# Kernel optimization log

Measured on AMD Instinct MI355X. Metric: run time of the kernel, lower is better.

## Reference

```python
import jax, jax.numpy as jnp
import numpy as np

H = 16        # num_attention_heads
D = 128       # head_dim
HID = 2048    # hidden_size
S = 2048      # seq_len
B = 2
EPS = 1.1920928955078125e-07  # torch.finfo(float32).eps, F.rms_norm default


def _rope(x, cos, sin):
    # x: [B,H,S,D]; cos/sin: [S, D//2] broadcast over B,H
    d = x.shape[-1] // 2
    x1, x2 = x[..., :d], x[..., d:]
    return jnp.concatenate([x1 * cos + x2 * sin, -x1 * sin + x2 * cos], axis=-1)


def _rmsnorm(x):
    ms = jnp.mean(x * x, axis=-1, keepdims=True)
    return x * jax.lax.rsqrt(ms + EPS)


def setup_inputs() -> dict:
    key = jax.random.key(0)
    ks = jax.random.split(key, 7)
    x = jax.random.normal(ks[0], (B, S, HID), dtype=jnp.float32)
    cos = jax.random.uniform(ks[1], (S, D // 2), dtype=jnp.float32)
    sin = jax.random.uniform(ks[2], (S, D // 2), dtype=jnp.float32)
    sc = 1.0 / np.sqrt(HID)
    wq = jax.random.normal(ks[3], (H * D, HID), dtype=jnp.float32) * sc
    wk = jax.random.normal(ks[4], (D, HID), dtype=jnp.float32) * sc  # num_kv_heads=1
    wv = jax.random.normal(ks[5], (D, HID), dtype=jnp.float32) * sc
    wo = jax.random.normal(ks[6], (HID, H * D), dtype=jnp.float32) * sc
    return {"x": x, "cos": cos, "sin": sin, "wq": wq, "wk": wk, "wv": wv, "wo": wo}


def reference(x, cos, sin, wq, wk, wv, wo):
    b, s, _ = x.shape
    # projections
    q = (x @ wq.T).reshape(b, s, H, D).transpose(0, 2, 1, 3)        # [b,H,s,D]
    k = (x @ wk.T).reshape(b, s, 1, D).transpose(0, 2, 1, 3)        # [b,1,s,D] MQA
    v = (x @ wv.T).reshape(b, s, 1, D).transpose(0, 2, 1, 3)
    # RoPE then RMS-norm on q/k (keep k/v in MQA [b,1,s,D]; broadcasting replaces expand)
    q = _rmsnorm(_rope(q, cos, sin))
    k = _rmsnorm(_rope(k, cos, sin))
    # causal attention
    scores = jnp.einsum('bhqd,bgkd->bhqk', q, k) * (D ** -0.5)      # [b,H,s,s]
    mask = jnp.tril(jnp.ones((s, s), dtype=bool))
    scores = jnp.where(mask, scores, -jnp.inf)
    attn = jax.nn.softmax(scores, axis=-1)
    out = jnp.einsum('bhqk,bgkd->bhqd', attn, v)                    # [b,H,s,D]
    out = out.transpose(0, 2, 1, 3).reshape(b, s, H * D)
    return out @ wo.T
```

## Files before the change

### kernel.cpp

```cpp
#include <hip/hip_runtime.h>
#include <hip/hip_bf16.h>

typedef __attribute__((ext_vector_type(8))) short bf16x8;
typedef __attribute__((ext_vector_type(4))) float f32x4;

constexpr int cH = 16, cD = 128, cHID = 2048, cS = 2048, cB = 2;
constexpr float cEPS = 1.1920928955078125e-07f;
constexpr float cQS = 0.08838834764831845f * 1.442695040888963f;

__device__ __forceinline__ unsigned short f2bf(float f) {
  union { float f; unsigned u; } v; v.f = f;
  unsigned r = v.u + 0x7fffu + ((v.u >> 16) & 1u);
  return (unsigned short)(r >> 16);
}
__device__ __forceinline__ unsigned pk2(float a, float b) {
  return (unsigned)f2bf(a) | ((unsigned)f2bf(b) << 16);
}
__device__ __forceinline__ f32x4 mfma16(bf16x8 a, bf16x8 b, f32x4 c) {
  return __builtin_amdgcn_mfma_f32_16x16x32_bf16(a, b, c, 0, 0, 0);
}
__device__ __forceinline__ void gl2l(const void* g, void* l) {
  __builtin_amdgcn_global_load_lds(
      (const __attribute__((address_space(1))) unsigned int*)g,
      (__attribute__((address_space(3))) unsigned int*)l, 16, 0, 0);
}

__global__ __launch_bounds__(256) void cvt_all(
    const float* __restrict__ x, const float* __restrict__ wq,
    const float* __restrict__ wk, const float* __restrict__ wv,
    const float* __restrict__ wo,
    unsigned short* __restrict__ xb, unsigned short* __restrict__ wqb,
    unsigned short* __restrict__ wkb, unsigned short* __restrict__ wvb,
    unsigned short* __restrict__ wob)
{
  long i = (long)blockIdx.x * 2048 + threadIdx.x * 8;
  const float* s; unsigned short* d; long off;
  if (i < 8388608)       { s = x;  d = xb;  off = i; }
  else if (i < 12582912) { s = wq; d = wqb; off = i - 8388608; }
  else if (i < 12845056) { s = wk; d = wkb; off = i - 12582912; }
  else if (i < 13107200) { s = wv; d = wvb; off = i - 12845056; }
  else                   { s = wo; d = wob; off = i - 13107200; }
  float4 v0 = *reinterpret_cast<const float4*>(s + off);
  float4 v1 = *reinterpret_cast<const float4*>(s + off + 4);
  uint4 o; o.x = pk2(v0.x, v0.y); o.y = pk2(v0.z, v0.w);
  o.z = pk2(v1.x, v1.y); o.w = pk2(v1.z, v1.w);
  *reinterpret_cast<uint4*>(d + off) = o;
}

__global__ __launch_bounds__(256) void gemm_qkv(
    const unsigned short* __restrict__ A,
    const unsigned short* __restrict__ Wq,
    const unsigned short* __restrict__ Wk,
    const unsigned short* __restrict__ Wv,
    const float* __restrict__ cosb, const float* __restrict__ sinb,
    unsigned short* __restrict__ Qn,
    unsigned short* __restrict__ Kn,
    unsigned short* __restrict__ Vn)
{
  __shared__ unsigned short lds[8192];
  const int t = threadIdx.x;
  const int bm = blockIdx.x, bn = blockIdx.y;
  const int lane = t & 63, w = t >> 6;
  const int hi = lane >> 4, l15 = lane & 15;

  const unsigned short* Wp; long wbase;
  if (bn < 16)       { Wp = Wq; wbase = (long)bn * 128; }
  else if (bn == 16) { Wp = Wk; wbase = 0; }
  else               { Wp = Wv; wbase = 0; }

  f32x4 acc[2][8] = {};

  for (int k0 = 0; k0 < 2048; k0 += 32) {
    #pragma unroll
    for (int i = 0; i < 2; ++i) {
      int c = w + 4 * i;
      gl2l(A + (long)(bm * 128 + 16 * c + (lane >> 2)) * 2048 + k0 + (lane & 3) * 8,
           &lds[c * 512]);
      gl2l(Wp + (wbase + 16 * c + (lane >> 2)) * 2048 + k0 + (lane & 3) * 8,
           &lds[4096 + c * 512]);
    }
    __syncthreads();
    bf16x8 af[2], bff[8];
    #pragma unroll
    for (int m = 0; m < 2; ++m)
      af[m] = *reinterpret_cast<const bf16x8*>(&lds[(w * 32 + m * 16 + l15) * 32 + hi * 8]);
    #pragma unroll
    for (int n = 0; n < 8; ++n)
      bff[n] = *reinterpret_cast<const bf16x8*>(&lds[4096 + (n * 16 + l15) * 32 + hi * 8]);
    #pragma unroll
    for (int m = 0; m < 2; ++m)
      #pragma unroll
      for (int n = 0; n < 8; ++n)
        acc[m][n] = mfma16(af[m], bff[n], acc[m][n]);
    __syncthreads();
  }

  const int rowbase = bm * 128 + w * 32;
  if (bn == 17) {
    #pragma unroll
    for (int m = 0; m < 2; ++m)
      #pragma unroll
      for (int r = 0; r < 4; ++r) {
        int grow = rowbase + m * 16 + hi * 4 + r;
        int b = grow >> 11, s = grow & 2047;
        long base = ((long)b * cS + s) * cD;
        #pragma unroll
        for (int n = 0; n < 8; ++n)
          Vn[base + n * 16 + l15] = f2bf(acc[m][n][r]);
      }
  } else {
    #pragma unroll
    for (int m = 0; m < 2; ++m)
      #pragma unroll
      for (int r = 0; r < 4; ++r) {
        int grow = rowbase + m * 16 + hi * 4 + r;
        int b = grow >> 11, s = grow & 2047;
        float o1[4], o2[4], ss = 0.f;
        #pragma unroll
        for (int n = 0; n < 4; ++n) {
          float cv = cosb[(long)s * 64 + n * 16 + l15];
          float sv = sinb[(long)s * 64 + n * 16 + l15];
          float x1 = acc[m][n][r], x2 = acc[m][n + 4][r];
          o1[n] = x1 * cv + x2 * sv;
          o2[n] = x2 * cv - x1 * sv;
          ss += o1[n] * o1[n] + o2[n] * o2[n];
        }
        ss += __shfl_xor(ss, 1); ss += __shfl_xor(ss, 2);
        ss += __shfl_xor(ss, 4); ss += __shfl_xor(ss, 8);
        float scn = rsqrtf(ss * (1.0f / 128.0f) + cEPS);
        if (bn < 16) {
          float sq = scn * cQS;
          long base = (((long)b * cH + bn) * cS + s) * cD;
          #pragma unroll
          for (int n = 0; n < 4; ++n) {
            Qn[base + n * 16 + l15] = f2bf(o1[n] * sq);
            Qn[base + 64 + n * 16 + l15] = f2bf(o2[n] * sq);
          }
        } else {
          long base = ((long)b * cS + s) * cD;
          int xs = (s & 7) << 3;
          #pragma unroll
          for (int n = 0; n < 4; ++n) {
            Kn[base + ((n * 16 + l15) ^ xs)] = f2bf(o1[n] * scn);
            Kn[base + (((64 + n * 16 + l15)) ^ xs)] = f2bf(o2[n] * scn);
          }
        }
      }
  }
}

__global__ __launch_bounds__(256) void vtrans(
    const unsigned short* __restrict__ Vn, unsigned short* __restrict__ Vt)
{
  __shared__ unsigned short Tl[64][72];
  const int t = threadIdx.x;
  const int st = blockIdx.x * 64, dt = blockIdx.y * 64, b = blockIdx.z;
  const unsigned short* Vb = Vn + (long)b * cS * cD;
  #pragma unroll
  for (int i = 0; i < 2; ++i) {
    int r = i * 32 + (t >> 3), c8 = (t & 7) * 8;
    *reinterpret_cast<uint4*>(&Tl[r][c8]) =
        *reinterpret_cast<const uint4*>(&Vb[(long)(st + r) * cD + dt + c8]);
  }
  __syncthreads();
  unsigned short* Vo = Vt + (long)b * cD * cS;
  #pragma unroll
  for (int i = 0; i < 2; ++i) {
    int d = i * 32 + (t >> 3), sb = (t & 7) * 8;
    unsigned short e[8];
    #pragma unroll
    for (int j = 0; j < 8; ++j) e[j] = Tl[sb + j][d];
    uint4 o;
    o.x = (unsigned)e[0] | ((unsigned)e[1] << 16);
    o.y = (unsigned)e[2] | ((unsigned)e[3] << 16);
    o.z = (unsigned)e[4] | ((unsigned)e[5] << 16);
    o.w = (unsigned)e[6] | ((unsigned)e[7] << 16);
    int dg = dt + d;
    *reinterpret_cast<uint4*>(&Vo[(long)dg * cS + st + (sb ^ ((dg & 7) << 3))]) = o;
  }
}

__global__ __launch_bounds__(256) void attn2(
    const unsigned short* __restrict__ Qn,
    const unsigned short* __restrict__ Kn,
    const unsigned short* __restrict__ Vt,
    unsigned short* __restrict__ O)
{
  __shared__ unsigned short lds[32768];
  const int t = threadIdx.x, w = t >> 6, lane = t & 63;
  const int hi = lane >> 4, l15 = lane & 15;
  const int h = blockIdx.y, b = blockIdx.z;
  const unsigned short* Qb = Qn + (long)(b * cH + h) * cS * cD;
  const unsigned short* Kb = Kn + (long)b * cS * cD;
  const unsigned short* Vtb = Vt + (long)b * cD * cS;
  const int x3 = (l15 & 7) << 3;

  union OU { unsigned u[4]; bf16x8 v; };
  OU ou; ou.u[0] = ou.u[1] = ou.u[2] = ou.u[3] = 0x3F803F80u;
  const bf16x8 onesv = ou.v;

  #pragma unroll 1
  for (int pass = 0; pass < 2; ++pass) {
    const int qt = (pass == 0) ? blockIdx.x : 31 - blockIdx.x;
    const int q0 = qt * 64;
    const int qrow = q0 + w * 16 + l15;
    const int nt = qt + 1;

    bf16x8 qf[4];
    #pragma unroll
    for (int kc = 0; kc < 4; ++kc)
      qf[kc] = *reinterpret_cast<const bf16x8*>(&Qb[(long)qrow * cD + kc * 32 + hi * 8]);

    const unsigned short* kp = Kb + (long)(16 * w + (lane >> 4)) * cD + (lane & 15) * 8;
    const unsigned short* vp[4];
    #pragma unroll
    for (int i = 0; i < 4; ++i)
      vp[i] = Vtb + (long)(32 * w + 8 * i + (lane >> 3)) * cS + (lane & 7) * 8;

    auto STAGE = [&](int buf) {
      unsigned short* kd = &lds[buf * 8192 + w * 2048];
      unsigned short* vd = &lds[16384 + buf * 8192 + w * 2048];
      #pragma unroll
      for (int i = 0; i < 4; ++i) {
        gl2l(kp + i * 512, kd + i * 512);
        gl2l(vp[i], vd + i * 512);
      }
      kp += 8192;
      #pragma unroll
      for (int i = 0; i < 4; ++i) vp[i] += 64;
    };

    f32x4 oacc[8] = {};
    f32x4 lacc = {};
    float mrun = -1e30f;

    STAGE(0);
    int cur = 0;

    #pragma unroll 1
    for (int kt = 0; kt < nt; ++kt) {
      const int kv0 = kt * 64;
      if (kt + 1 < nt) {
        STAGE(cur ^ 1);
        asm volatile("s_waitcnt vmcnt(8)" ::: "memory");
      } else {
        asm volatile("s_waitcnt vmcnt(0)" ::: "memory");
      }
      __builtin_amdgcn_s_barrier();
      __builtin_amdgcn_sched_barrier(0);

      const unsigned short* kbase = &lds[cur * 8192];
      const unsigned short* vbase = &lds[16384 + cur * 8192];

      f32x4 st[4] = {};
      #pragma unroll
      for (int kc = 0; kc < 4; ++kc) {
        #pragma unroll
        for (int n = 0; n < 4; ++n) {
          bf16x8 kf = *reinterpret_cast<const bf16x8*>(
              &kbase[(n * 16 + l15) * 128 + ((kc * 32 + hi * 8) ^ x3)]);
          st[n] = mfma16(kf, qf[kc], st[n]);
        }
      }

      float p[4][4];
      if (kt == qt) {
        #pragma unroll
        for (int n = 0; n < 4; ++n)
          #pragma unroll
          for (int r = 0; r < 4; ++r) {
            int kv = kv0 + n * 16 + hi * 4 + r;
            p[n][r] = (kv <= qrow) ? st[n][r] : -1e30f;
          }
      } else {
        #pragma unroll
        for (int n = 0; n < 4; ++n)
          #pragma unroll
          for (int r = 0; r < 4; ++r)
            p[n][r] = st[n][r];
      }

      float pmax = p[0][0];
      #pragma unroll
      for (int n = 0; n < 4; ++n)
        #pragma unroll
        for (int r = 0; r < 4; ++r) pmax = fmaxf(pmax, p[n][r]);
      pmax = fmaxf(pmax, __shfl_xor(pmax, 16));
      pmax = fmaxf(pmax, __shfl_xor(pmax, 32));

      if (!__all(pmax - mrun <= 8.0f)) {
        float mnew = fmaxf(mrun, pmax);
        float alpha = exp2f(mrun - mnew);
        mrun = mnew;
        #pragma unroll
        for (int n = 0; n < 8; ++n)
          #pragma unroll
          for (int r = 0; r < 4; ++r) oacc[n][r] *= alpha;
        #pragma unroll
        for (int r = 0; r < 4; ++r) lacc[r] *= alpha;
      }

      #pragma unroll
      for (int n = 0; n < 4; ++n)
        #pragma unroll
        for (int r = 0; r < 4; ++r)
          p[n][r] = exp2f(p[n][r] - mrun);

      unsigned pkl[4], pkh[4];
      #pragma unroll
      for (int n = 0; n < 4; ++n) {
        pkl[n] = pk2(p[n][0], p[n][1]);
        pkh[n] = pk2(p[n][2], p[n][3]);
      }

      bf16x8 pa[2];
      #pragma unroll
      for (int c = 0; c < 2; ++c) {
        int ns = 2 * c + (hi >> 1);
        int no = 2 * c + ((hi >> 1) ^ 1);
        unsigned own0 = pkl[ns], own1 = pkh[ns];
        unsigned ot0 = pkl[no], ot1 = pkh[no];
        unsigned a160 = __shfl_xor(own0, 16), a161 = __shfl_xor(own1, 16);
        unsigned a320 = __shfl_xor(ot0, 32),  a321 = __shfl_xor(ot1, 32);
        unsigned a480 = __shfl_xor(ot0, 48),  a481 = __shfl_xor(ot1, 48);
        unsigned w0 = hi == 0 ? own0 : hi == 1 ? a480 : hi == 2 ? a320 : a160;
        unsigned w1 = hi == 0 ? own1 : hi == 1 ? a481 : hi == 2 ? a321 : a161;
        unsigned w2 = hi == 0 ? a160 : hi == 1 ? a320 : hi == 2 ? a480 : own0;
        unsigned w3 = hi == 0 ? a161 : hi == 1 ? a321 : hi == 2 ? a481 : own1;
        union { unsigned u[4]; bf16x8 v; } cvt;
        cvt.u[0] = w0; cvt.u[1] = w1; cvt.u[2] = w2; cvt.u[3] = w3;
        pa[c] = cvt.v;
      }

      #pragma unroll
      for (int c = 0; c < 2; ++c) lacc = mfma16(onesv, pa[c], lacc);
      #pragma unroll
      for (int n2 = 0; n2 < 8; ++n2) {
        #pragma unroll
        for (int c = 0; c < 2; ++c) {
          bf16x8 vf = *reinterpret_cast<const bf16x8*>(
              &vbase[(n2 * 16 + l15) * 64 + ((c * 32 + hi * 8) ^ x3)]);
          oacc[n2] = mfma16(vf, pa[c], oacc[n2]);
        }
      }
      __builtin_amdgcn_s_barrier();
      cur ^= 1;
    }

    {
      float inv = 1.0f / lacc[0];
      unsigned short* Ol = &lds[w * 2176];
      #pragma unroll
      for (int n2 = 0; n2 < 8; ++n2)
        #pragma unroll
        for (int r = 0; r < 4; ++r)
          Ol[l15 * 136 + n2 * 16 + hi * 4 + r] = f2bf(oacc[n2][r] * inv);
      __syncthreads();
      #pragma unroll
      for (int i = 0; i < 4; ++i) {
        int row = hi + 4 * i;
        uint4 ov = *reinterpret_cast<const uint4*>(&Ol[row * 136 + l15 * 8]);
        *reinterpret_cast<uint4*>(
            &O[(long)(b * cS + q0 + w * 16 + row) * (cH * cD) + h * cD + l15 * 8]) = ov;
      }
      __syncthreads();
    }
  }
}

__global__ __launch_bounds__(256) void gemm_out(
    const unsigned short* __restrict__ A,
    const unsigned short* __restrict__ W,
    float* __restrict__ C)
{
  __shared__ unsigned short lds[8192];
  const int t = threadIdx.x;
  const int bm = blockIdx.x, bn = blockIdx.y;
  const int lane = t & 63, w = t >> 6;
  const int wr = w >> 1, wc = w & 1, hi = lane >> 4, l15 = lane & 15;
  const long wbase = (long)bn * 128;

  f32x4 acc[4][4] = {};
  for (int k0 = 0; k0 < 2048; k0 += 32) {
    #pragma unroll
    for (int i = 0; i < 2; ++i) {
      int c = w + 4 * i;
      gl2l(A + (long)(bm * 128 + 16 * c + (lane >> 2)) * 2048 + k0 + (lane & 3) * 8,
           &lds[c * 512]);
      gl2l(W + (wbase + 16 * c + (lane >> 2)) * 2048 + k0 + (lane & 3) * 8,
           &lds[4096 + c * 512]);
    }
    __syncthreads();
    bf16x8 af[4], bff[4];
    #pragma unroll
    for (int m = 0; m < 4; ++m)
      af[m] = *reinterpret_cast<const bf16x8*>(&lds[(wr * 64 + m * 16 + l15) * 32 + hi * 8]);
    #pragma unroll
    for (int n = 0; n < 4; ++n)
      bff[n] = *reinterpret_cast<const bf16x8*>(&lds[4096 + (wc * 64 + n * 16 + l15) * 32 + hi * 8]);
    #pragma unroll
    for (int m = 0; m < 4; ++m)
      #pragma unroll
      for (int n = 0; n < 4; ++n)
        acc[m][n] = mfma16(af[m], bff[n], acc[m][n]);
    __syncthreads();
  }

  #pragma unroll
  for (int m = 0; m < 4; ++m) {
    int row = bm * 128 + wr * 64 + m * 16 + hi * 4;
    #pragma unroll
    for (int n = 0; n < 4; ++n) {
      int col = bn * 128 + wc * 64 + n * 16 + l15;
      #pragma unroll
      for (int r = 0; r < 4; ++r)
        C[(long)(row + r) * 2048 + col] = acc[m][n][r];
    }
  }
}

extern "C" void kernel_launch(void* const* d_in, const int* in_sizes, int n_in,
                              void* d_out, int out_size, void* d_ws, size_t ws_size,
                              hipStream_t stream) {
  const float* x    = (const float*)d_in[0];
  const float* cosb = (const float*)d_in[1];
  const float* sinb = (const float*)d_in[2];
  const float* wq   = (const float*)d_in[3];
  const float* wk   = (const float*)d_in[4];
  const float* wv   = (const float*)d_in[5];
  const float* wo   = (const float*)d_in[6];
  float* out = (float*)d_out;

  char* ws = (char*)d_ws;
  unsigned short* xb  = (unsigned short*)(ws);
  unsigned short* wqb = (unsigned short*)(ws + 16777216);
  unsigned short* wkb = (unsigned short*)(ws + 25165824);
  unsigned short* wvb = (unsigned short*)(ws + 25690112);
  unsigned short* Qn  = (unsigned short*)(ws + 26214400);
  unsigned short* Kn  = (unsigned short*)(ws + 42991616);
  unsigned short* Vn  = (unsigned short*)(ws + 44040192);
  unsigned short* Vtg = (unsigned short*)(ws + 45088768);
  unsigned short* wob = (unsigned short*)(ws + 46137344);
  unsigned short* Ob  = (unsigned short*)ws;

  cvt_all<<<dim3(8448), 256, 0, stream>>>(x, wq, wk, wv, wo, xb, wqb, wkb, wvb, wob);
  gemm_qkv<<<dim3(32, 18), 256, 0, stream>>>(xb, wqb, wkb, wvb, cosb, sinb, Qn, Kn, Vn);
  vtrans<<<dim3(32, 2, 2), 256, 0, stream>>>(Vn, Vtg);
  attn2<<<dim3(16, 16, 2), 256, 0, stream>>>(Qn, Kn, Vtg, Ob);
  gemm_out<<<dim3(32, 16), 256, 0, stream>>>(Ob, wob, out);
}
```

Measured before the change: 207.1 us.

## Use 16x16x16 bf16 MFMA for PV to skip P cross-lane shuffles

Replaces the PV and row-sum MFMAs with the K=16 bf16 variant so the softmax probabilities already held in each lane's score layout can feed the MFMA directly, removing the shuffle-and-select exchange of packed P. Packs P with the hardware v_cvt_pk_bf16_f32 instruction instead of software rounding. Also defers the cross-lane max reduction to the rescale branch and raises wave priority around the MFMA blocks. Doubles the MFMA instruction count for PV with smaller V fragment loads, and the deferred max changes which max is used per lane only when rescaling is skipped.

```diff
diff --git a/kernel.cpp b/kernel.cpp
--- a/kernel.cpp
+++ b/kernel.cpp
@@ -2,6 +2,7 @@
 #include <hip/hip_bf16.h>
 
 typedef __attribute__((ext_vector_type(8))) short bf16x8;
+typedef __attribute__((ext_vector_type(4))) short bf16x4;
 typedef __attribute__((ext_vector_type(4))) float f32x4;
 
 constexpr int cH = 16, cD = 128, cHID = 2048, cS = 2048, cB = 2;
@@ -16,8 +17,23 @@
 __device__ __forceinline__ unsigned pk2(float a, float b) {
   return (unsigned)f2bf(a) | ((unsigned)f2bf(b) << 16);
 }
+__device__ __forceinline__ unsigned cvtpk(float a, float b) {
+  unsigned r;
+  asm("v_cvt_pk_bf16_f32 %0, %1, %2" : "=v"(r) : "v"(a), "v"(b));
+  return r;
+}
 __device__ __forceinline__ f32x4 mfma16(bf16x8 a, bf16x8 b, f32x4 c) {
   return __builtin_amdgcn_mfma_f32_16x16x32_bf16(a, b, c, 0, 0, 0);
+}
+__device__ __forceinline__ f32x4 mfma16k16(bf16x4 a, bf16x4 b, f32x4 c) {
+#if __has_builtin(__builtin_amdgcn_mfma_f32_16x16x16bf16_1k)
+  return __builtin_amdgcn_mfma_f32_16x16x16bf16_1k(a, b, c, 0, 0, 0);
+#else
+  f32x4 d;
+  asm volatile("v_mfma_f32_16x16x16_bf16 %0, %1, %2, %3\n\ts_nop 7\n\ts_nop 2"
+               : "=v"(d) : "v"(a), "v"(b), "v"(c));
+  return d;
+#endif
 }
 __device__ __forceinline__ void gl2l(const void* g, void* l) {
   __builtin_amdgcn_global_load_lds(
@@ -195,9 +211,9 @@
   const unsigned short* Vtb = Vt + (long)b * cD * cS;
   const int x3 = (l15 & 7) << 3;
 
-  union OU { unsigned u[4]; bf16x8 v; };
-  OU ou; ou.u[0] = ou.u[1] = ou.u[2] = ou.u[3] = 0x3F803F80u;
-  const bf16x8 onesv = ou.v;
+  union O4 { unsigned u[2]; bf16x4 v; };
+  O4 o4; o4.u[0] = o4.u[1] = 0x3F803F80u;
+  const bf16x4 ones4 = o4.v;
 
   #pragma unroll 1
   for (int pass = 0; pass < 2; ++pass) {
@@ -253,6 +269,7 @@
       const unsigned short* vbase = &lds[16384 + cur * 8192];
 
       f32x4 st[4] = {};
+      __builtin_amdgcn_s_setprio(1);
       #pragma unroll
       for (int kc = 0; kc < 4; ++kc) {
         #pragma unroll
@@ -262,6 +279,7 @@
           st[n] = mfma16(kf, qf[kc], st[n]);
         }
       }
+      __builtin_amdgcn_s_setprio(0);
 
       float p[4][4];
       if (kt == qt) {
@@ -280,15 +298,15 @@
             p[n][r] = st[n][r];
       }
 
-      float pmax = p[0][0];
-      #pragma unroll
-      for (int n = 0; n < 4; ++n)
-        #pragma unroll
-        for (int r = 0; r < 4; ++r) pmax = fmaxf(pmax, p[n][r]);
-      pmax = fmaxf(pmax, __shfl_xor(pmax, 16));
-      pmax = fmaxf(pmax, __shfl_xor(pmax, 32));
+      float t0 = fmaxf(fmaxf(p[0][0], p[0][1]), fmaxf(p[0][2], p[0][3]));
+      float t1 = fmaxf(fmaxf(p[1][0], p[1][1]), fmaxf(p[1][2], p[1][3]));
+      float t2 = fmaxf(fmaxf(p[2][0], p[2][1]), fmaxf(p[2][2], p[2][3]));
+      float t3 = fmaxf(fmaxf(p[3][0], p[3][1]), fmaxf(p[3][2], p[3][3]));
+      float pmax = fmaxf(fmaxf(t0, t1), fmaxf(t2, t3));
 
       if (!__all(pmax - mrun <= 8.0f)) {
+        pmax = fmaxf(pmax, __shfl_xor(pmax, 16));
+        pmax = fmaxf(pmax, __shfl_xor(pmax, 32));
         float mnew = fmaxf(mrun, pmax);
         float alpha = exp2f(mrun - mnew);
         mrun = mnew;
@@ -306,43 +324,28 @@
         for (int r = 0; r < 4; ++r)
           p[n][r] = exp2f(p[n][r] - mrun);
 
-      unsigned pkl[4], pkh[4];
+      bf16x4 paB[4];
       #pragma unroll
       for (int n = 0; n < 4; ++n) {
-        pkl[n] = pk2(p[n][0], p[n][1]);
-        pkh[n] = pk2(p[n][2], p[n][3]);
-      }
-
-      bf16x8 pa[2];
-      #pragma unroll
-      for (int c = 0; c < 2; ++c) {
-        int ns = 2 * c + (hi >> 1);
-        int no = 2 * c + ((hi >> 1) ^ 1);
-        unsigned own0 = pkl[ns], own1 = pkh[ns];
-        unsigned ot0 = pkl[no], ot1 = pkh[no];
-        unsigned a160 = __shfl_xor(own0, 16), a161 = __shfl_xor(own1, 16);
-        unsigned a320 = __shfl_xor(ot0, 32),  a321 = __shfl_xor(ot1, 32);
-        unsigned a480 = __shfl_xor(ot0, 48),  a481 = __shfl_xor(ot1, 48);
-        unsigned w0 = hi == 0 ? own0 : hi == 1 ? a480 : hi == 2 ? a320 : a160;
-        unsigned w1 = hi == 0 ? own1 : hi == 1 ? a481 : hi == 2 ? a321 : a161;
-        unsigned w2 = hi == 0 ? a160 : hi == 1 ? a320 : hi == 2 ? a480 : own0;
-        unsigned w3 = hi == 0 ? a161 : hi == 1 ? a321 : hi == 2 ? a481 : own1;
-        union { unsigned u[4]; bf16x8 v; } cvt;
-        cvt.u[0] = w0; cvt.u[1] = w1; cvt.u[2] = w2; cvt.u[3] = w3;
-        pa[c] = cvt.v;
-      }
-
-      #pragma unroll
-      for (int c = 0; c < 2; ++c) lacc = mfma16(onesv, pa[c], lacc);
+        O4 pu;
+        pu.u[0] = cvtpk(p[n][0], p[n][1]);
+        pu.u[1] = cvtpk(p[n][2], p[n][3]);
+        paB[n] = pu.v;
+      }
+
+      __builtin_amdgcn_s_setprio(1);
+      #pragma unroll
+      for (int n = 0; n < 4; ++n) lacc = mfma16k16(ones4, paB[n], lacc);
       #pragma unroll
       for (int n2 = 0; n2 < 8; ++n2) {
         #pragma unroll
-        for (int c = 0; c < 2; ++c) {
-          bf16x8 vf = *reinterpret_cast<const bf16x8*>(
-              &vbase[(n2 * 16 + l15) * 64 + ((c * 32 + hi * 8) ^ x3)]);
-          oacc[n2] = mfma16(vf, pa[c], oacc[n2]);
+        for (int n = 0; n < 4; ++n) {
+          bf16x4 vf = *reinterpret_cast<const bf16x4*>(
+              &vbase[(n2 * 16 + l15) * 64 + ((n * 16 + hi * 4) ^ x3)]);
+          oacc[n2] = mfma16k16(vf, paB[n], oacc[n2]);
         }
       }
+      __builtin_amdgcn_s_setprio(0);
       __builtin_amdgcn_s_barrier();
       cur ^= 1;
     }
```

New measurement: 204.2 us. About the same (-1.4%).
